# Kernel tuning notes

Hardware: AMD Instinct MI355X
Metric: run time of the kernel (lower is better)

## Reference

```python
import jax, jax.numpy as jnp
import numpy as np

B, S, D = 4, 2048, 1024
MAG_SCALE = 5.0


def setup_inputs() -> dict:
    key = jax.random.key(0)
    ks = jax.random.split(key, 16)
    sd = 1.0 / np.sqrt(D)  # keep pre-activations O(1)
    inp = {
        "x": jax.random.normal(ks[0], (B, S, D), jnp.float32),
        "W_omega": jax.random.normal(ks[1], (D, D), jnp.float32) * sd,
        "b_omega": jnp.zeros((D,), jnp.float32),
        "W_mag": jax.random.normal(ks[2], (D, D), jnp.float32) * sd,
        "b_mag": jnp.zeros((D,), jnp.float32),
        "W_phi0": jax.random.normal(ks[3], (D, D), jnp.float32) * sd,
        "b_phi0": jnp.zeros((D,), jnp.float32),
        "W_gate": jax.random.normal(ks[4], (D, D), jnp.float32) * sd,
        "b_gate": jnp.zeros((D,), jnp.float32),
        "W_q": jax.random.normal(ks[5], (D, D), jnp.float32) * sd,
        "b_q": jnp.zeros((D,), jnp.float32),
        "integration_scale": jax.random.uniform(ks[6], (D,), jnp.float32),
        "W_out": jax.random.normal(ks[7], (4 * D, D), jnp.float32) * (1.0 / np.sqrt(4 * D)),
        "b_out": jnp.zeros((D,), jnp.float32),
    }
    return inp


def reference(x, W_omega, b_omega, W_mag, b_mag, W_phi0, b_phi0,
              W_gate, b_gate, W_q, b_q, integration_scale, W_out, b_out):
    lin = lambda h, W, b: h @ W + b  # [B,S,*] @ [*,Dout]

    omega = lin(x, W_omega, b_omega)                      # phase velocity [B,S,D]
    magnitude = jax.nn.sigmoid(lin(x, W_mag, b_mag)) * MAG_SCALE
    gate = jax.nn.sigmoid(lin(x, W_gate, b_gate))
    gated_omega = gate * (omega * jnp.abs(integration_scale))
    phi = lin(x, W_phi0, b_phi0) + jnp.cumsum(gated_omega, axis=1)  # integrated phase

    cos_phi = jnp.cos(phi)
    sin_phi = jnp.sin(phi)

    # holographic memory write: cumulative complex binding of content with phase
    weighted_content = magnitude * x
    memory_real = jnp.cumsum(weighted_content * cos_phi, axis=1)
    memory_imag = jnp.cumsum(weighted_content * sin_phi, axis=1)
    sqrt_mag = jnp.sqrt(jnp.cumsum(magnitude, axis=1) + 1e-8)
    memory_real = memory_real / sqrt_mag
    memory_imag = memory_imag / sqrt_mag

    # complex retrieval at a query phase
    phi_q = phi + lin(x, W_q, b_q)
    cos_q, sin_q = jnp.cos(phi_q), jnp.sin(phi_q)
    retrieved_real = memory_real * cos_q + memory_imag * sin_q
    retrieved_imag = memory_imag * cos_q - memory_real * sin_q

    context = jnp.concatenate(
        [x * cos_phi, x * sin_phi, retrieved_real, retrieved_imag], axis=-1)  # [B,S,4D]
    return x + lin(context, W_out, b_out)


if __name__ == "__main__":
    out = reference(**setup_inputs())
    print(out.shape, out.dtype)
```

## Files before the change

### kernel.cpp

```cpp
#include <hip/hip_runtime.h>
#include <hip/hip_fp16.h>

#define B_ 4
#define S_ 2048
#define D_ 1024
#define CCH 64
#define LCH 32
#define NELEM ((size_t)B_*S_*D_)
#define MROWS (B_*S_)

typedef __attribute__((ext_vector_type(4))) float f32x4;
typedef __attribute__((ext_vector_type(8))) _Float16 f16x8;

__device__ __forceinline__ ushort f2h(float v) {
  __half h = __float2half(v);
  return __builtin_bit_cast(ushort, h);
}
__device__ __forceinline__ float h2f(ushort u) {
  return __half2float(__builtin_bit_cast(__half, u));
}

__device__ __forceinline__ void gload16(const ushort* src, char* ldsdst) {
  __builtin_amdgcn_global_load_lds(
      (const __attribute__((address_space(1))) void*)src,
      (__attribute__((address_space(3))) void*)ldsdst, 16, 0, 0);
}


__global__ void xhalf_kernel(const float* __restrict__ x, ushort* __restrict__ xh) {
  size_t i = ((size_t)blockIdx.x * blockDim.x + threadIdx.x) * 8;
  if (i >= NELEM) return;
  float4 a = *(const float4*)(x + i);
  float4 b = *(const float4*)(x + i + 4);
  ushort h[8] = {f2h(a.x), f2h(a.y), f2h(a.z), f2h(a.w),
                 f2h(b.x), f2h(b.y), f2h(b.z), f2h(b.w)};
  *(ushort4*)(xh + i) = *(ushort4*)h;
  *(ushort4*)(xh + i + 4) = *(ushort4*)(h + 4);
}

__global__ void transpose5(const float* __restrict__ W0, const float* __restrict__ W1,
                           const float* __restrict__ W2, const float* __restrict__ W3,
                           const float* __restrict__ W4, ushort* __restrict__ Th) {
  __shared__ float tile[64][65];
  const int z = blockIdx.z;
  const float* W = (z == 0) ? W0 : (z == 1) ? W1 : (z == 2) ? W2 : (z == 3) ? W3 : W4;
  ushort* T = Th + (size_t)z * D_ * D_;
  const int k0 = blockIdx.x * 64, n0 = blockIdx.y * 64;
  const int tx = threadIdx.x & 63, ty = threadIdx.x >> 6;
#pragma unroll
  for (int i = 0; i < 16; ++i)
    tile[ty * 16 + i][tx] = W[(size_t)(k0 + ty * 16 + i) * D_ + n0 + tx];
  __syncthreads();
#pragma unroll
  for (int i = 0; i < 16; ++i) {
    const int nn = ty * 16 + i;
    T[(size_t)(n0 + nn) * D_ + k0 + tx] = f2h(tile[tx][nn]);
  }
}

__global__ void transpose_convert(const float* __restrict__ W, ushort* __restrict__ Th, int sh,
                                  int Kd, int Nd) {
  __shared__ float tile[64][65];
  const int k0 = blockIdx.x * 64, n0 = blockIdx.y * 64;
  const int tx = threadIdx.x & 63, ty = threadIdx.x >> 6;
#pragma unroll
  for (int i = 0; i < 16; ++i)
    tile[ty * 16 + i][tx] = W[(size_t)(k0 + ty * 16 + i) * Nd + n0 + tx];
  __syncthreads();
#pragma unroll
  for (int i = 0; i < 16; ++i) {
    const int nn = ty * 16 + i;
    Th[(size_t)(n0 + nn) * sh + k0 + tx] = f2h(tile[tx][nn]);
  }
}

template <int FINAL, int SPLITK>
__global__ __launch_bounds__(512, 2) void gemm256(
    const ushort* __restrict__ A, int lda, const ushort* __restrict__ Bw,
    ushort* __restrict__ Ch, ushort* __restrict__ C4h,
    float* __restrict__ Cf, float* __restrict__ C4f,
    const float* __restrict__ xres, const float* __restrict__ bias,
    int M, int K) {
  __shared__ __align__(16) char ldsc[4 * 32768];
  int bid = blockIdx.x, ks = 0;
  if (SPLITK && bid >= 128) { ks = 1; bid -= 128; }
  const int tm = bid & 31, tn = bid >> 5;
  const int Kb = SPLITK ? (K >> 1) : K;
  const int ldb = K;
  const int nB = tn << 8;
  if (SPLITK) { A += (size_t)ks * Kb; Bw += (size_t)ks * Kb; }
  const int NT = Kb >> 5;
  const int t = threadIdx.x, lane = t & 63, wid = t >> 6;
  const int wm = wid >> 2, wn = wid & 3;

  f32x4 acc[8][4];
#pragma unroll
  for (int i = 0; i < 8; ++i)
#pragma unroll
    for (int j = 0; j < 4; ++j) acc[i][j] = (f32x4){0.f, 0.f, 0.f, 0.f};

  const int line1 = t >> 3;
  const int g8s = (t & 7) ^ (line1 & 7);
  const int rowS = line1 * 2 + (g8s >> 2);
  const int kgS = (g8s & 3) << 3;
  const ushort* srcA = A + (size_t)(tm * 256 + rowS) * lda + kgS;
  const ushort* srcB = Bw + (size_t)(nB + rowS) * ldb + kgS;
  char* dstA = ldsc + (size_t)t * 16;
  char* dstB = ldsc + 16384 + (size_t)t * 16;

  auto STAGE = [&](int tile) {
    const int ts = (tile < NT) ? tile : NT - 1;
    char* ba = dstA + (tile & 3) * 32768;
    char* bb = dstB + (tile & 3) * 32768;
    const ushort* sa = srcA + ts * 32;
    const ushort* sb = srcB + ts * 32;
    gload16(sa, ba);
    gload16(sa + (size_t)128 * lda, ba + 8192);
    gload16(sb, bb);
    gload16(sb + (size_t)128 * ldb, bb + 8192);
  };

  const int lane15 = lane & 15;
  const int hl = lane15 >> 1;
  const int swz = ((((lane15 & 1) << 2) + (lane >> 4)) ^ hl) << 4;
  const char* aB = ldsc + wm * 8192 + hl * 128 + swz;
  const char* bB = ldsc + 16384 + wn * 4096 + hl * 128 + swz;

  STAGE(0); STAGE(1); STAGE(2);
  asm volatile("s_waitcnt vmcnt(8)" ::: "memory");
  __builtin_amdgcn_sched_barrier(0);
  __builtin_amdgcn_s_barrier();

#pragma unroll 1
  for (int tt = 0; tt < NT; ++tt) {
    STAGE(tt + 3);
    const char* ab = aB + (tt & 3) * 32768;
    const char* bb = bB + (tt & 3) * 32768;
    f16x8 af[4], bf_[4], af2[4];
#pragma unroll
    for (int f = 0; f < 4; ++f) af[f] = *(const f16x8*)(ab + f * 1024);
#pragma unroll
    for (int c = 0; c < 4; ++c) bf_[c] = *(const f16x8*)(bb + c * 1024);
#pragma unroll
    for (int f = 0; f < 4; ++f) af2[f] = *(const f16x8*)(ab + 4096 + f * 1024);
    asm volatile("s_waitcnt lgkmcnt(4)" ::: "memory");
    __builtin_amdgcn_sched_barrier(0);
    __builtin_amdgcn_s_setprio(1);
#pragma unroll
    for (int f = 0; f < 4; ++f)
#pragma unroll
      for (int c = 0; c < 4; ++c)
        acc[f][c] = __builtin_amdgcn_mfma_f32_16x16x32_f16(af[f], bf_[c], acc[f][c], 0, 0, 0);
    __builtin_amdgcn_s_setprio(0);
    asm volatile("s_waitcnt lgkmcnt(0)" ::: "memory");
    __builtin_amdgcn_sched_barrier(0);
    __builtin_amdgcn_s_setprio(1);
#pragma unroll
    for (int f = 0; f < 4; ++f)
#pragma unroll
      for (int c = 0; c < 4; ++c)
        acc[4 + f][c] = __builtin_amdgcn_mfma_f32_16x16x32_f16(af2[f], bf_[c], acc[4 + f][c], 0, 0, 0);
    __builtin_amdgcn_s_setprio(0);
    asm volatile("s_waitcnt vmcnt(8)" ::: "memory");
    __builtin_amdgcn_sched_barrier(0);
    __builtin_amdgcn_s_barrier();
  }

#pragma unroll
  for (int i = 0; i < 8; ++i) {
    const int row0 = tm * 256 + wm * 128 + i * 16 + ((lane >> 4) << 2);
#pragma unroll
    for (int jj = 0; jj < 4; ++jj) {
      const int col = tn * 256 + wn * 64 + jj * 16 + lane15;
      if (SPLITK && ks) {
#pragma unroll
        for (int r = 0; r < 4; ++r)
          C4f[(size_t)(row0 + r) * 1024 + col] = acc[i][jj][r];
      } else if (FINAL) {
#pragma unroll
        for (int r = 0; r < 4; ++r) {
          const size_t idx = (size_t)(row0 + r) * 1024 + col;
          Cf[idx] = acc[i][jj][r] + xres[idx] + bias[col];
        }
      } else {
        const int pl = col >> 10;
        ushort* base = (pl < 4) ? (Ch + (size_t)pl * (size_t)M * 1024) : C4h;
#pragma unroll
        for (int r = 0; r < 4; ++r)
          base[(size_t)(row0 + r) * 1024 + (col & 1023)] = f2h(acc[i][jj][r]);
      }
    }
  }
}

__global__ void add_kernel(float* __restrict__ out, const float* __restrict__ p) {
  size_t i = ((size_t)blockIdx.x * blockDim.x + threadIdx.x) * 4;
  if (i >= NELEM) return;
  float4 a = *(const float4*)(out + i);
  float4 b = *(const float4*)(p + i);
  a.x += b.x; a.y += b.y; a.z += b.z; a.w += b.w;
  *(float4*)(out + i) = a;
}


__device__ __forceinline__ void load4h(const ushort* p, float* f) {
  ushort4 u = *(const ushort4*)p;
  f[0] = h2f(u.x); f[1] = h2f(u.y); f[2] = h2f(u.z); f[3] = h2f(u.w);
}

__global__ void prep_chunk_kernel(ushort* __restrict__ omega_go, const ushort* __restrict__ gate_lin,
                                  ushort* __restrict__ mag_io,
                                  const float* __restrict__ b_om, const float* __restrict__ b_gate,
                                  const float* __restrict__ b_mag, const float* __restrict__ isc,
                                  float* __restrict__ gsum, float* __restrict__ msum) {
  int tid = blockIdx.x * blockDim.x + threadIdx.x;
  if (tid >= B_ * CCH * (D_ / 4)) return;
  int d4 = tid & 255, c = (tid >> 8) & (CCH - 1), b = tid >> 14;
  int d = d4 * 4;
  size_t base = ((size_t)(b * S_) + c * LCH) * D_ + d;
  size_t cs = ((size_t)(b * CCH) + c) * D_ + d;
  float bo[4], bg[4], bm[4], is[4];
  *(float4*)bo = *(const float4*)(b_om + d);
  *(float4*)bg = *(const float4*)(b_gate + d);
  *(float4*)bm = *(const float4*)(b_mag + d);
  *(float4*)is = *(const float4*)(isc + d);
  float sg[4] = {0.f, 0.f, 0.f, 0.f}, sm[4] = {0.f, 0.f, 0.f, 0.f};
  for (int s = 0; s < LCH; ++s) {
    size_t i = base + (size_t)s * D_;
    float om[4], gl[4], mg[4];
    load4h(omega_go + i, om);
    load4h(gate_lin + i, gl);
    load4h(mag_io + i, mg);
    ushort wo[4], wm_[4];
#pragma unroll
    for (int j = 0; j < 4; ++j) {
      float g = 1.f / (1.f + __expf(-(gl[j] + bg[j])));
      float m5 = 5.f / (1.f + __expf(-(mg[j] + bm[j])));
      float go = g * ((om[j] + bo[j]) * fabsf(is[j]));
      sg[j] += go;
      sm[j] += m5;
      wo[j] = f2h(go);
      wm_[j] = f2h(m5);
    }
    *(ushort4*)(omega_go + i) = *(ushort4*)wo;
    *(ushort4*)(mag_io + i) = *(ushort4*)wm_;
  }
  *(float4*)(gsum + cs) = *(float4*)sg;
  *(float4*)(msum + cs) = *(float4*)sm;
}

__global__ void scan_offsets_kernel(float* __restrict__ s1, float* __restrict__ s2) {
  int gw = (blockIdx.x * blockDim.x + threadIdx.x) >> 6;
  int lane = threadIdx.x & 63;
  if (gw >= B_ * D_) return;
  int d = gw & (D_ - 1), b = gw >> 10;
  size_t idx = ((size_t)(b * CCH) + lane) * D_ + d;
  float v1 = s1[idx], v2 = s2[idx];
#pragma unroll
  for (int off = 1; off < 64; off <<= 1) {
    float u1 = __shfl_up(v1, off);
    float u2 = __shfl_up(v2, off);
    if (lane >= off) { v1 += u1; v2 += u2; }
  }
  float e1 = __shfl_up(v1, 1), e2 = __shfl_up(v2, 1);
  if (lane == 0) { e1 = 0.f; e2 = 0.f; }
  s1[idx] = e1;
  s2[idx] = e2;
}

__global__ void phase_scan_kernel(const ushort* __restrict__ xh, const ushort* __restrict__ go,
                                  const ushort* __restrict__ mag, const ushort* __restrict__ p0,
                                  const float* __restrict__ goff,
                                  float* __restrict__ trsum, float* __restrict__ tisum,
                                  const float* __restrict__ b_phi, ushort* __restrict__ ctx) {
  int tid = blockIdx.x * blockDim.x + threadIdx.x;
  if (tid >= B_ * CCH * (D_ / 4)) return;
  int d4 = tid & 255, c = (tid >> 8) & (CCH - 1), b = tid >> 14;
  int d = d4 * 4;
  size_t base = ((size_t)(b * S_) + c * LCH) * D_ + d;
  size_t cs = ((size_t)(b * CCH) + c) * D_ + d;
  float pr[4], bp[4];
  *(float4*)pr = *(const float4*)(goff + cs);
  *(float4*)bp = *(const float4*)(b_phi + d);
  float tr[4] = {0.f, 0.f, 0.f, 0.f}, ti[4] = {0.f, 0.f, 0.f, 0.f};
  size_t crow = ((size_t)(b * S_ + c * LCH)) * 4096 + d;
  for (int s = 0; s < LCH; ++s) {
    size_t i = base + (size_t)s * D_;
    float g[4], ph0[4], m[4], xv[4];
    load4h(go + i, g);
    load4h(p0 + i, ph0);
    load4h(mag + i, m);
    load4h(xh + i, xv);
    ushort c4[4], s4[4];
#pragma unroll
    for (int j = 0; j < 4; ++j) {
      pr[j] += g[j];
      float ph = ph0[j] + bp[j] + pr[j];
      float sp, cp;
      __sincosf(ph, &sp, &cp);
      float wr = m[j] * xv[j];
      tr[j] += wr * cp;
      ti[j] += wr * sp;
      c4[j] = f2h(xv[j] * cp);
      s4[j] = f2h(xv[j] * sp);
    }
    *(ushort4*)(ctx + crow) = *(ushort4*)c4;
    *(ushort4*)(ctx + crow + 1024) = *(ushort4*)s4;
    crow += 4096;
  }
  *(float4*)(trsum + cs) = *(float4*)tr;
  *(float4*)(tisum + cs) = *(float4*)ti;
}

__global__ void retrieve_kernel(const ushort* __restrict__ xh, const ushort* __restrict__ go,
                                const ushort* __restrict__ mag, const ushort* __restrict__ p0,
                                const ushort* __restrict__ q,
                                const float* __restrict__ goff, const float* __restrict__ moff,
                                const float* __restrict__ troff, const float* __restrict__ tioff,
                                const float* __restrict__ b_phi, const float* __restrict__ b_q,
                                ushort* __restrict__ ctx) {
  int tid = blockIdx.x * blockDim.x + threadIdx.x;
  if (tid >= B_ * CCH * (D_ / 4)) return;
  int d4 = tid & 255, c = (tid >> 8) & (CCH - 1), b = tid >> 14;
  int d = d4 * 4;
  size_t base = ((size_t)(b * S_) + c * LCH) * D_ + d;
  size_t cs = ((size_t)(b * CCH) + c) * D_ + d;
  float pr[4], mr[4], tr[4], ti[4], bp[4], bq[4];
  *(float4*)pr = *(const float4*)(goff + cs);
  *(float4*)mr = *(const float4*)(moff + cs);
  *(float4*)tr = *(const float4*)(troff + cs);
  *(float4*)ti = *(const float4*)(tioff + cs);
  *(float4*)bp = *(const float4*)(b_phi + d);
  *(float4*)bq = *(const float4*)(b_q + d);
  size_t crow = ((size_t)(b * S_ + c * LCH)) * 4096 + d;
  for (int s = 0; s < LCH; ++s) {
    size_t i = base + (size_t)s * D_;
    float g[4], ph0[4], m[4], xv[4], qv[4];
    load4h(go + i, g);
    load4h(p0 + i, ph0);
    load4h(mag + i, m);
    load4h(q + i, qv);
    load4h(xh + i, xv);
    ushort r2[4], r3[4];
#pragma unroll
    for (int j = 0; j < 4; ++j) {
      pr[j] += g[j];
      float ph = ph0[j] + bp[j] + pr[j];
      float sp, cp;
      __sincosf(ph, &sp, &cp);
      mr[j] += m[j];
      float wr = m[j] * xv[j];
      tr[j] += wr * cp;
      ti[j] += wr * sp;
      float rs = rsqrtf(mr[j] + 1e-8f);
      float mreal = tr[j] * rs, mimag = ti[j] * rs;
      float phq = ph + qv[j] + bq[j];
      float sq, cq;
      __sincosf(phq, &sq, &cq);
      r2[j] = f2h(mreal * cq + mimag * sq);
      r3[j] = f2h(mimag * cq - mreal * sq);
    }
    *(ushort4*)(ctx + crow + 2048) = *(ushort4*)r2;
    *(ushort4*)(ctx + crow + 3072) = *(ushort4*)r3;
    crow += 4096;
  }
}

extern "C" void kernel_launch(void* const* d_in, const int* in_sizes, int n_in,
                              void* d_out, int out_size, void* d_ws, size_t ws_size,
                              hipStream_t stream) {
  const float* x      = (const float*)d_in[0];
  const float* W_om   = (const float*)d_in[1];
  const float* b_om   = (const float*)d_in[2];
  const float* W_mag  = (const float*)d_in[3];
  const float* b_mag  = (const float*)d_in[4];
  const float* W_phi  = (const float*)d_in[5];
  const float* b_phi  = (const float*)d_in[6];
  const float* W_gate = (const float*)d_in[7];
  const float* b_gate = (const float*)d_in[8];
  const float* W_q    = (const float*)d_in[9];
  const float* b_q    = (const float*)d_in[10];
  const float* isc    = (const float*)d_in[11];
  const float* W_out  = (const float*)d_in[12];
  const float* b_out  = (const float*)d_in[13];
  float* out = (float*)d_out;

  const size_t WS_NEEDED = 213909504ull;
  if (ws_size < WS_NEEDED) {
    (void)hipMemsetAsync(d_out, 0, (size_t)out_size * sizeof(float), stream);
    return;
  }
  char* w = (char*)d_ws;
  ushort* planes_h = (ushort*)w;
  ushort* omega_buf = planes_h;
  ushort* gate_buf  = planes_h + NELEM;
  ushort* mag_buf   = planes_h + 2 * NELEM;
  ushort* phi0_buf  = planes_h + 3 * NELEM;
  float* partial    = (float*)w;
  ushort* x_h   = (ushort*)(w + 67108864);
  ushort* q_buf = (ushort*)out;
  char* ctxb = w + 4 * NELEM * 4;
  ushort* ctx   = (ushort*)ctxb;
  ushort* W5T   = (ushort*)(ctxb + 16777216);
  ushort* WoutT = (ushort*)(w + 201326592);
  float* gsum  = (float*)(w + 209715200);
  float* msum  = (float*)(w + 210763776);
  float* trsum = (float*)(w + 211812352);
  float* tisum = (float*)(w + 212860928);

  const size_t DD = (size_t)D_ * D_;

  xhalf_kernel<<<(int)(NELEM / 2048), 256, 0, stream>>>(x, x_h);
  transpose5<<<dim3(16, 16, 5), 256, 0, stream>>>(W_om, W_gate, W_mag, W_phi, W_q, W5T);
  transpose_convert<<<dim3(64, 16), 256, 0, stream>>>(W_out, WoutT, 4096, 4 * D_, D_);

  gemm256<0, 0><<<640, 512, 0, stream>>>(x_h, 1024, W5T, planes_h, q_buf,
                                         nullptr, nullptr, nullptr, nullptr, MROWS, 1024);

  prep_chunk_kernel<<<B_ * CCH * (D_ / 4) / 256, 256, 0, stream>>>(
      omega_buf, gate_buf, mag_buf, b_om, b_gate, b_mag, isc, gsum, msum);
  scan_offsets_kernel<<<B_ * D_ * 64 / 256, 256, 0, stream>>>(gsum, msum);
  phase_scan_kernel<<<B_ * CCH * (D_ / 4) / 256, 256, 0, stream>>>(
      x_h, omega_buf, mag_buf, phi0_buf, gsum, trsum, tisum, b_phi, ctx);
  scan_offsets_kernel<<<B_ * D_ * 64 / 256, 256, 0, stream>>>(trsum, tisum);
  retrieve_kernel<<<B_ * CCH * (D_ / 4) / 256, 256, 0, stream>>>(
      x_h, omega_buf, mag_buf, phi0_buf, q_buf, gsum, msum, trsum, tisum, b_phi, b_q, ctx);

  gemm256<1, 1><<<256, 512, 0, stream>>>(ctx, 4096, WoutT, nullptr, nullptr, out, partial,
                                         x, b_out, MROWS, 4 * D_);
  add_kernel<<<(int)(NELEM / 1024), 256, 0, stream>>>(out, partial);
}
```

Baseline: 317.3 us.

## Shrink GEMM tile to 128x256 with triple buffering and drop split-K

Replaces the 256x256-tile GEMM with a 128x256 tile, cutting per-thread accumulators in half and moving from a 4-slot to a 3-slot LDS ring. The output projection no longer uses split-K, so the fp32 partial buffer write and the separate add kernel go away, and the grid still gives 256 blocks. The first projection GEMM now launches 1280 blocks instead of 640. In exchange each tile reuses less data, the prefetch depth is shallower, and the long K=4096 loop now runs in each block without being split.

Result: faster. 291.1 us (-8.2%).

```diff
diff --git a/kernel.cpp b/kernel.cpp
--- a/kernel.cpp
+++ b/kernel.cpp
@@ -74,28 +74,23 @@
   }
 }
 
-template <int FINAL, int SPLITK>
-__global__ __launch_bounds__(512, 2) void gemm256(
+template <int FINAL>
+__global__ __launch_bounds__(512, 2) void gemm128(
     const ushort* __restrict__ A, int lda, const ushort* __restrict__ Bw,
     ushort* __restrict__ Ch, ushort* __restrict__ C4h,
-    float* __restrict__ Cf, float* __restrict__ C4f,
-    const float* __restrict__ xres, const float* __restrict__ bias,
+    float* __restrict__ Cf, const float* __restrict__ xres, const float* __restrict__ bias,
     int M, int K) {
-  __shared__ __align__(16) char ldsc[4 * 32768];
-  int bid = blockIdx.x, ks = 0;
-  if (SPLITK && bid >= 128) { ks = 1; bid -= 128; }
-  const int tm = bid & 31, tn = bid >> 5;
-  const int Kb = SPLITK ? (K >> 1) : K;
+  __shared__ __align__(16) char ldsc[3 * 24576];
+  const int bid = blockIdx.x;
+  const int tm = bid & 63, tn = bid >> 6;
   const int ldb = K;
-  const int nB = tn << 8;
-  if (SPLITK) { A += (size_t)ks * Kb; Bw += (size_t)ks * Kb; }
-  const int NT = Kb >> 5;
+  const int NT = K >> 5;
   const int t = threadIdx.x, lane = t & 63, wid = t >> 6;
   const int wm = wid >> 2, wn = wid & 3;
 
-  f32x4 acc[8][4];
-#pragma unroll
-  for (int i = 0; i < 8; ++i)
+  f32x4 acc[4][4];
+#pragma unroll
+  for (int i = 0; i < 4; ++i)
 #pragma unroll
     for (int j = 0; j < 4; ++j) acc[i][j] = (f32x4){0.f, 0.f, 0.f, 0.f};
 
@@ -103,19 +98,18 @@
   const int g8s = (t & 7) ^ (line1 & 7);
   const int rowS = line1 * 2 + (g8s >> 2);
   const int kgS = (g8s & 3) << 3;
-  const ushort* srcA = A + (size_t)(tm * 256 + rowS) * lda + kgS;
-  const ushort* srcB = Bw + (size_t)(nB + rowS) * ldb + kgS;
+  const ushort* srcA = A + (size_t)(tm * 128 + rowS) * lda + kgS;
+  const ushort* srcB = Bw + (size_t)(tn * 256 + rowS) * ldb + kgS;
   char* dstA = ldsc + (size_t)t * 16;
-  char* dstB = ldsc + 16384 + (size_t)t * 16;
-
-  auto STAGE = [&](int tile) {
+  char* dstB = ldsc + 8192 + (size_t)t * 16;
+
+  auto STAGE = [&](int tile, int slot) {
     const int ts = (tile < NT) ? tile : NT - 1;
-    char* ba = dstA + (tile & 3) * 32768;
-    char* bb = dstB + (tile & 3) * 32768;
+    char* ba = dstA + slot * 24576;
+    char* bb = dstB + slot * 24576;
     const ushort* sa = srcA + ts * 32;
     const ushort* sb = srcB + ts * 32;
     gload16(sa, ba);
-    gload16(sa + (size_t)128 * lda, ba + 8192);
     gload16(sb, bb);
     gload16(sb + (size_t)128 * ldb, bb + 8192);
   };
@@ -123,27 +117,26 @@
   const int lane15 = lane & 15;
   const int hl = lane15 >> 1;
   const int swz = ((((lane15 & 1) << 2) + (lane >> 4)) ^ hl) << 4;
-  const char* aB = ldsc + wm * 8192 + hl * 128 + swz;
-  const char* bB = ldsc + 16384 + wn * 4096 + hl * 128 + swz;
-
-  STAGE(0); STAGE(1); STAGE(2);
-  asm volatile("s_waitcnt vmcnt(8)" ::: "memory");
+  const char* aB = ldsc + wm * 4096 + hl * 128 + swz;
+  const char* bB = ldsc + 8192 + wn * 4096 + hl * 128 + swz;
+
+  STAGE(0, 0); STAGE(1, 1);
+  asm volatile("s_waitcnt vmcnt(3)" ::: "memory");
   __builtin_amdgcn_sched_barrier(0);
   __builtin_amdgcn_s_barrier();
 
+  int s_rd = 0, s_st = 2;
 #pragma unroll 1
   for (int tt = 0; tt < NT; ++tt) {
-    STAGE(tt + 3);
-    const char* ab = aB + (tt & 3) * 32768;
-    const char* bb = bB + (tt & 3) * 32768;
-    f16x8 af[4], bf_[4], af2[4];
+    STAGE(tt + 2, s_st);
+    const char* ab = aB + s_rd * 24576;
+    const char* bb = bB + s_rd * 24576;
+    f16x8 af[4], bf_[4];
 #pragma unroll
     for (int f = 0; f < 4; ++f) af[f] = *(const f16x8*)(ab + f * 1024);
 #pragma unroll
     for (int c = 0; c < 4; ++c) bf_[c] = *(const f16x8*)(bb + c * 1024);
-#pragma unroll
-    for (int f = 0; f < 4; ++f) af2[f] = *(const f16x8*)(ab + 4096 + f * 1024);
-    asm volatile("s_waitcnt lgkmcnt(4)" ::: "memory");
+    asm volatile("s_waitcnt lgkmcnt(0)" ::: "memory");
     __builtin_amdgcn_sched_barrier(0);
     __builtin_amdgcn_s_setprio(1);
 #pragma unroll
@@ -152,31 +145,20 @@
       for (int c = 0; c < 4; ++c)
         acc[f][c] = __builtin_amdgcn_mfma_f32_16x16x32_f16(af[f], bf_[c], acc[f][c], 0, 0, 0);
     __builtin_amdgcn_s_setprio(0);
-    asm volatile("s_waitcnt lgkmcnt(0)" ::: "memory");
-    __builtin_amdgcn_sched_barrier(0);
-    __builtin_amdgcn_s_setprio(1);
-#pragma unroll
-    for (int f = 0; f < 4; ++f)
-#pragma unroll
-      for (int c = 0; c < 4; ++c)
-        acc[4 + f][c] = __builtin_amdgcn_mfma_f32_16x16x32_f16(af2[f], bf_[c], acc[4 + f][c], 0, 0, 0);
-    __builtin_amdgcn_s_setprio(0);
-    asm volatile("s_waitcnt vmcnt(8)" ::: "memory");
+    asm volatile("s_waitcnt vmcnt(3)" ::: "memory");
     __builtin_amdgcn_sched_barrier(0);
     __builtin_amdgcn_s_barrier();
-  }
-
-#pragma unroll
-  for (int i = 0; i < 8; ++i) {
-    const int row0 = tm * 256 + wm * 128 + i * 16 + ((lane >> 4) << 2);
+    s_rd = (s_rd == 2) ? 0 : s_rd + 1;
+    s_st = (s_st == 2) ? 0 : s_st + 1;
+  }
+
+#pragma unroll
+  for (int i = 0; i < 4; ++i) {
+    const int row0 = tm * 128 + wm * 64 + i * 16 + ((lane >> 4) << 2);
 #pragma unroll
     for (int jj = 0; jj < 4; ++jj) {
       const int col = tn * 256 + wn * 64 + jj * 16 + lane15;
-      if (SPLITK && ks) {
-#pragma unroll
-        for (int r = 0; r < 4; ++r)
-          C4f[(size_t)(row0 + r) * 1024 + col] = acc[i][jj][r];
-      } else if (FINAL) {
+      if (FINAL) {
 #pragma unroll
         for (int r = 0; r < 4; ++r) {
           const size_t idx = (size_t)(row0 + r) * 1024 + col;
@@ -191,15 +173,6 @@
       }
     }
   }
-}
-
-__global__ void add_kernel(float* __restrict__ out, const float* __restrict__ p) {
-  size_t i = ((size_t)blockIdx.x * blockDim.x + threadIdx.x) * 4;
-  if (i >= NELEM) return;
-  float4 a = *(const float4*)(out + i);
-  float4 b = *(const float4*)(p + i);
-  a.x += b.x; a.y += b.y; a.z += b.z; a.w += b.w;
-  *(float4*)(out + i) = a;
 }
 
 
@@ -396,7 +369,6 @@
   ushort* gate_buf  = planes_h + NELEM;
   ushort* mag_buf   = planes_h + 2 * NELEM;
   ushort* phi0_buf  = planes_h + 3 * NELEM;
-  float* partial    = (float*)w;
   ushort* x_h   = (ushort*)(w + 67108864);
   ushort* q_buf = (ushort*)out;
   char* ctxb = w + 4 * NELEM * 4;
@@ -408,14 +380,12 @@
   float* trsum = (float*)(w + 211812352);
   float* tisum = (float*)(w + 212860928);
 
-  const size_t DD = (size_t)D_ * D_;
-
   xhalf_kernel<<<(int)(NELEM / 2048), 256, 0, stream>>>(x, x_h);
   transpose5<<<dim3(16, 16, 5), 256, 0, stream>>>(W_om, W_gate, W_mag, W_phi, W_q, W5T);
   transpose_convert<<<dim3(64, 16), 256, 0, stream>>>(W_out, WoutT, 4096, 4 * D_, D_);
 
-  gemm256<0, 0><<<640, 512, 0, stream>>>(x_h, 1024, W5T, planes_h, q_buf,
-                                         nullptr, nullptr, nullptr, nullptr, MROWS, 1024);
+  gemm128<0><<<1280, 512, 0, stream>>>(x_h, 1024, W5T, planes_h, q_buf,
+                                       nullptr, nullptr, nullptr, MROWS, 1024);
 
   prep_chunk_kernel<<<B_ * CCH * (D_ / 4) / 256, 256, 0, stream>>>(
       omega_buf, gate_buf, mag_buf, b_om, b_gate, b_mag, isc, gsum, msum);
@@ -426,7 +396,6 @@
   retrieve_kernel<<<B_ * CCH * (D_ / 4) / 256, 256, 0, stream>>>(
       x_h, omega_buf, mag_buf, phi0_buf, q_buf, gsum, msum, trsum, tisum, b_phi, b_q, ctx);
 
-  gemm256<1, 1><<<256, 512, 0, stream>>>(ctx, 4096, WoutT, nullptr, nullptr, out, partial,
-                                         x, b_out, MROWS, 4 * D_);
-  add_kernel<<<(int)(NELEM / 1024), 256, 0, stream>>>(out, partial);
-}
+  gemm128<1><<<256, 512, 0, stream>>>(ctx, 4096, WoutT, nullptr, nullptr, out,
+                                      x, b_out, MROWS, 4 * D_);
+}
```
